# Optimization experiments

Hardware: AMD Instinct MI355X
Metric: run time of the kernel (lower is better)

The kernel has to match this reference:

```python
import jax, jax.numpy as jnp
import numpy as np

B, CIN, T = 32, 64, 4096
E, H, HD, FF, L = 256, 8, 32, 1024, 4
K, S = 15, 2
SEQ = 512
GROUPS = E // 2
EPS = 1e-5


def setup_inputs() -> dict:
    key = jax.random.key(0)
    ks = jax.random.split(key, 16)
    d = {}
    d['x'] = jax.random.normal(ks[0], (B, CIN, T), jnp.float32)
    d['conv0_w'] = jax.random.normal(ks[1], (E, CIN, K), jnp.float32) * 0.03
    d['conv0_b'] = jnp.zeros((E,), jnp.float32)
    d['conv12_w'] = jax.random.normal(ks[2], (2, E, E, K), jnp.float32) * 0.016
    d['conv12_b'] = jnp.zeros((2, E), jnp.float32)
    d['gn_g'] = jnp.ones((3, E), jnp.float32)
    d['gn_b'] = jnp.zeros((3, E), jnp.float32)
    d['Wq'] = jax.random.normal(ks[3], (L, H, HD, E), jnp.float32) * 0.0625
    d['Wk'] = jax.random.normal(ks[4], (L, H, HD, E), jnp.float32) * 0.0625
    d['Wv'] = jax.random.normal(ks[5], (L, H, HD, E), jnp.float32) * 0.0625
    d['Wo'] = jax.random.normal(ks[6], (L, E, E), jnp.float32) * 0.0625
    d['ln1_g'] = jnp.ones((L, E), jnp.float32)
    d['ln1_b'] = jnp.zeros((L, E), jnp.float32)
    d['Wf1'] = jax.random.normal(ks[7], (L, FF, E), jnp.float32) * 0.0625
    d['bf1'] = jnp.zeros((L, FF), jnp.float32)
    d['Wf2'] = jax.random.normal(ks[8], (L, E, FF), jnp.float32) * 0.03125
    d['bf2'] = jnp.zeros((L, E), jnp.float32)
    d['ln2_g'] = jnp.ones((L, E), jnp.float32)
    d['ln2_b'] = jnp.zeros((L, E), jnp.float32)
    d['Wc1'] = jax.random.normal(ks[9], (256, SEQ * E), jnp.float32) * 0.003
    d['bc1'] = jnp.zeros((256,), jnp.float32)
    d['Wc2'] = jax.random.normal(ks[10], (1, 256), jnp.float32) * 0.0625
    d['bc2'] = jnp.zeros((1,), jnp.float32)
    return d


def conv1d(x, w, b, stride, pad):
    y = jax.lax.conv_general_dilated(x, w, (stride,), [(pad, pad)],
                                     dimension_numbers=('NCH', 'OIH', 'NCH'))
    return y + b[None, :, None]


def group_norm(x, g, b):
    # x: [B, C, Len]; torch GroupNorm with C//2 groups
    Bn, C, Ln = x.shape
    xg = x.reshape(Bn, GROUPS, C // GROUPS, Ln)
    mu = xg.mean(axis=(2, 3), keepdims=True)
    var = ((xg - mu) ** 2).mean(axis=(2, 3), keepdims=True)
    xn = ((xg - mu) * jax.lax.rsqrt(var + EPS)).reshape(Bn, C, Ln)
    return xn * g[None, :, None] + b[None, :, None]


def layer_norm(x, g, b):
    mu = x.mean(-1, keepdims=True)
    var = ((x - mu) ** 2).mean(-1, keepdims=True)
    return (x - mu) * jax.lax.rsqrt(var + EPS) * g + b


def pos_encoding(seq, e):
    t = jnp.arange(seq, dtype=jnp.float32)[:, None]
    i = jnp.arange(e, dtype=jnp.float32)[None, :]
    ang = t / jnp.power(10000.0, i / e)  # note: i/e, matching the source
    return jnp.where(jnp.arange(e)[None, :] % 2 == 0, jnp.sin(ang), jnp.cos(ang))


def reference(x, conv0_w, conv0_b, conv12_w, conv12_b, gn_g, gn_b,
              Wq, Wk, Wv, Wo, ln1_g, ln1_b, Wf1, bf1, Wf2, bf2,
              ln2_g, ln2_b, Wc1, bc1, Wc2, bc2):
    # --- conv encoder: (conv -> dropout(eval) -> groupnorm -> gelu) x3 ---
    h = conv1d(x, conv0_w, conv0_b, S, K // 2)
    h = jax.nn.gelu(group_norm(h, gn_g[0], gn_b[0]), approximate=False)
    for i in range(2):
        h = conv1d(h, conv12_w[i], conv12_b[i], S, K // 2)
        h = jax.nn.gelu(group_norm(h, gn_g[i + 1], gn_b[i + 1]), approximate=False)
    h = jnp.transpose(h, (0, 2, 1))  # [B, SEQ, E]

    # --- transformer encoder ---
    h = h + pos_encoding(h.shape[1], E)[None]
    scale = 1.0 / jnp.sqrt(jnp.float32(HD))
    for l in range(L):
        q = jnp.einsum('bse,hde->bhsd', h, Wq[l])
        k = jnp.einsum('bse,hde->bhsd', h, Wk[l])
        v = jnp.einsum('bse,hde->bhsd', h, Wv[l])
        attn = jax.nn.softmax(jnp.einsum('bhqd,bhkd->bhqk', q, k) * scale, axis=-1)
        o = jnp.einsum('bhqk,bhkd->bhqd', attn, v)
        o = jnp.transpose(o, (0, 2, 1, 3)).reshape(h.shape[0], h.shape[1], E)
        o = o @ Wo[l].T
        h1 = layer_norm(o + h, ln1_g[l], ln1_b[l])
        f = jax.nn.relu(h1 @ Wf1[l].T + bf1[l]) @ Wf2[l].T + bf2[l]
        h = layer_norm(f + h1, ln2_g[l], ln2_b[l])

    # --- binary classifier ---
    flat = h.reshape(h.shape[0], -1)  # [B, SEQ*E]
    hid = jax.nn.relu(flat @ Wc1.T + bc1)
    return jax.nn.sigmoid(hid @ Wc2.T + bc2)  # [B, 1]
```

## Files before the change

### kernel.cpp

```cpp
#include <hip/hip_runtime.h>
#include <math.h>


typedef unsigned int   u32;
typedef unsigned short u16;
typedef __attribute__((ext_vector_type(4))) float f32x4;
typedef __attribute__((ext_vector_type(8))) short bf16x8;

#define QSCALE_LOG2E 0.2550348742f

__device__ __forceinline__ u16 f2bf(float v) {
    union { float f; u32 u; } x; x.f = v;
    u32 r = x.u + 0x7fffu + ((x.u >> 16) & 1u);
    return (u16)(r >> 16);
}

__device__ __forceinline__ void gl2lds16(const void* gsrc, void* ldst) {
    __builtin_amdgcn_global_load_lds(
        (const __attribute__((address_space(1))) void*)gsrc,
        (__attribute__((address_space(3))) void*)ldst, 16, 0, 0);
}

__device__ __forceinline__ float maeeg_block_sum(float v, float* sc4) {
#pragma unroll
    for (int off = 32; off; off >>= 1) v += __shfl_down(v, off);
    int t = threadIdx.x;
    if ((t & 63) == 0) sc4[t >> 6] = v;
    __syncthreads();
    float r = sc4[0] + sc4[1] + sc4[2] + sc4[3];
    __syncthreads();
    return r;
}

__global__ __launch_bounds__(256) void maeeg_mm_kernel(
    const u16* __restrict__ Ag, const u16* __restrict__ Bg,
    const float* __restrict__ bias, const float* __restrict__ res,
    void* __restrict__ outp, int N, int K, int flags)
{
    __shared__ u16 As[8192];
    __shared__ u16 Bs[8192];
    const int m0 = blockIdx.x * 128, n0 = blockIdx.y * 128;
    const int t = threadIdx.x, w = t >> 6, lane = t & 63;
    const int fr = lane & 15, fq = lane >> 4;
    const int wm = (w >> 1) * 64, wn = (w & 1) * 64;
    const int srow = lane >> 3;
    const int srcc = (lane & 7) ^ srow;

    f32x4 acc[4][4];
    const f32x4 zero = {0.f, 0.f, 0.f, 0.f};
#pragma unroll
    for (int i = 0; i < 4; ++i)
#pragma unroll
        for (int j = 0; j < 4; ++j) acc[i][j] = zero;

    for (int k0 = 0; k0 < K; k0 += 64) {
#pragma unroll
        for (int j = 0; j < 4; ++j) {
            int rowb = w * 32 + j * 8;
            int r = rowb + srow;
            gl2lds16(Ag + (size_t)(m0 + r) * K + k0 + srcc * 8,
                     (char*)As + rowb * 128);
            gl2lds16(Bg + (size_t)(n0 + r) * K + k0 + srcc * 8,
                     (char*)Bs + rowb * 128);
        }
        __syncthreads();
#pragma unroll
        for (int kc = 0; kc < 2; ++kc) {
            bf16x8 af[4], bfv[4];
#pragma unroll
            for (int i = 0; i < 4; ++i) {
                int am = wm + i * 16 + fr;
                int bn = wn + i * 16 + fr;
                int kb = kc * 64 + fq * 16;
                af[i]  = *(const bf16x8*)((const char*)As + am * 128 + (kb ^ ((am & 7) << 4)));
                bfv[i] = *(const bf16x8*)((const char*)Bs + bn * 128 + (kb ^ ((bn & 7) << 4)));
            }
#pragma unroll
            for (int i = 0; i < 4; ++i)
#pragma unroll
                for (int j = 0; j < 4; ++j)
                    acc[i][j] = __builtin_amdgcn_mfma_f32_16x16x32_bf16(
                        af[i], bfv[j], acc[i][j], 0, 0, 0);
        }
        __syncthreads();
    }
#pragma unroll
    for (int i = 0; i < 4; ++i) {
#pragma unroll
        for (int j = 0; j < 4; ++j) {
            int n = n0 + wn + j * 16 + fr;
            float bv = bias ? bias[n] : 0.f;
#pragma unroll
            for (int r = 0; r < 4; ++r) {
                int m = m0 + wm + i * 16 + fq * 4 + r;
                float v = acc[i][j][r] + bv;
                if (res) v += res[(size_t)m * N + n];
                if (flags & 1) v = fmaxf(v, 0.f);
                if (flags & 16) {
                    u16* o = (u16*)outp;
                    int seg = n >> 8, nn = n & 255;
                    if (seg == 0)
                        o[(size_t)m * 256 + nn] = f2bf(v * QSCALE_LOG2E);
                    else if (seg == 1)
                        o[4194304 + (size_t)m * 256 + nn] = f2bf(v);
                    else
                        o[8388608 + (((size_t)(m >> 9)) * 256 + nn) * 512 + (m & 511)] = f2bf(v);
                } else if (flags & 4)
                    ((u16*)outp)[(((size_t)(m >> 9)) * 256 + n) * 512 + (m & 511)] = f2bf(v);
                else if (flags & 2)
                    ((u16*)outp)[(size_t)m * N + n] = f2bf(v);
                else
                    ((float*)outp)[(size_t)m * N + n] = v;
            }
        }
    }
}

__global__ __launch_bounds__(512) void maeeg_mmln_kernel(
    const u16* __restrict__ Ag, const u16* __restrict__ Bg,
    const float* __restrict__ bias, const float* __restrict__ res,
    const float* __restrict__ g, const float* __restrict__ b,
    float* __restrict__ outf, u16* __restrict__ outb, int K)
{
    __shared__ u16 As[64 * 64];
    __shared__ u16 Bs[256 * 64];
    __shared__ float psum[64][4];
    __shared__ float psq[64][4];
    const int m0 = blockIdx.x * 64;
    const int t = threadIdx.x, w = t >> 6, lane = t & 63;
    const int fr = lane & 15, fq = lane >> 4;
    const int wm = (w & 1) * 32, wn = (w >> 1) * 64;
    const int seg = w >> 1;
    const int srow = lane >> 3;
    const int srcc = (lane & 7) ^ srow;

    f32x4 acc[2][4];
    const f32x4 zero = {0.f, 0.f, 0.f, 0.f};
#pragma unroll
    for (int i = 0; i < 2; ++i)
#pragma unroll
        for (int j = 0; j < 4; ++j) acc[i][j] = zero;

    for (int k0 = 0; k0 < K; k0 += 64) {
        gl2lds16(Ag + (size_t)(m0 + w * 8 + srow) * K + k0 + srcc * 8,
                 (char*)As + (w * 8) * 128);
#pragma unroll
        for (int j = 0; j < 4; ++j) {
            int rowb = w * 32 + j * 8;
            gl2lds16(Bg + (size_t)(rowb + srow) * K + k0 + srcc * 8,
                     (char*)Bs + rowb * 128);
        }
        __syncthreads();
#pragma unroll
        for (int kc = 0; kc < 2; ++kc) {
            int kb = kc * 64 + fq * 16;
            bf16x8 af[2], bfv[4];
#pragma unroll
            for (int i = 0; i < 2; ++i) {
                int am = wm + i * 16 + fr;
                af[i] = *(const bf16x8*)((const char*)As + am * 128 + (kb ^ ((am & 7) << 4)));
            }
#pragma unroll
            for (int j = 0; j < 4; ++j) {
                int bn = wn + j * 16 + fr;
                bfv[j] = *(const bf16x8*)((const char*)Bs + bn * 128 + (kb ^ ((bn & 7) << 4)));
            }
#pragma unroll
            for (int i = 0; i < 2; ++i)
#pragma unroll
                for (int j = 0; j < 4; ++j)
                    acc[i][j] = __builtin_amdgcn_mfma_f32_16x16x32_bf16(
                        af[i], bfv[j], acc[i][j], 0, 0, 0);
        }
        __syncthreads();
    }

#pragma unroll
    for (int j = 0; j < 4; ++j) {
        int n = wn + j * 16 + fr;
        float bv = bias ? bias[n] : 0.f;
#pragma unroll
        for (int i = 0; i < 2; ++i)
#pragma unroll
            for (int r = 0; r < 4; ++r) {
                int m = m0 + wm + i * 16 + fq * 4 + r;
                acc[i][j][r] += bv + res[(size_t)m * 256 + n];
            }
    }
#pragma unroll
    for (int i = 0; i < 2; ++i)
#pragma unroll
        for (int r = 0; r < 4; ++r) {
            float s = acc[i][0][r] + acc[i][1][r] + acc[i][2][r] + acc[i][3][r];
            float q = acc[i][0][r] * acc[i][0][r] + acc[i][1][r] * acc[i][1][r]
                    + acc[i][2][r] * acc[i][2][r] + acc[i][3][r] * acc[i][3][r];
#pragma unroll
            for (int off = 1; off < 16; off <<= 1) {
                s += __shfl_xor(s, off);
                q += __shfl_xor(q, off);
            }
            if (fr == 0) {
                int ml = wm + i * 16 + fq * 4 + r;
                psum[ml][seg] = s;
                psq[ml][seg] = q;
            }
        }
    __syncthreads();
#pragma unroll
    for (int i = 0; i < 2; ++i)
#pragma unroll
        for (int r = 0; r < 4; ++r) {
            int ml = wm + i * 16 + fq * 4 + r;
            float S = psum[ml][0] + psum[ml][1] + psum[ml][2] + psum[ml][3];
            float Q = psq[ml][0] + psq[ml][1] + psq[ml][2] + psq[ml][3];
            float mu = S * (1.f / 256.f);
            float var = fmaxf(Q * (1.f / 256.f) - mu * mu, 0.f);
            float rs = rsqrtf(var + 1e-5f);
            size_t mrow = (size_t)(m0 + ml) * 256;
#pragma unroll
            for (int j = 0; j < 4; ++j) {
                int n = wn + j * 16 + fr;
                float o = (acc[i][j][r] - mu) * rs * g[n] + b[n];
                if (outf) outf[mrow + n] = o;
                outb[mrow + n] = f2bf(o);
            }
        }
}

__global__ __launch_bounds__(256) void maeeg_convmm_kernel(
    const u16* __restrict__ Wp, const u16* __restrict__ inp,
    const float* __restrict__ cb, u16* __restrict__ out,
    int K3, int len_in, int len_out)
{
    __shared__ u16 As[8192];
    __shared__ u16 Bs[8192];
    const int m0 = blockIdx.x * 128, t0 = blockIdx.y * 128, b = blockIdx.z;
    const int lip = len_in + 16;
    const u16* inb = inp + (size_t)b * (K3 >> 4) * lip;
    const int t = threadIdx.x, w = t >> 6, lane = t & 63;
    const int sr = lane & 7, sc = lane >> 3;
    const int fr = lane & 15, fq = lane >> 4;
    const int wm = (w >> 1) * 64, wn = (w & 1) * 64;
    const int srow = lane >> 3;
    const int srcc = (lane & 7) ^ srow;

    f32x4 acc[4][4];
    const f32x4 zero = {0.f, 0.f, 0.f, 0.f};
#pragma unroll
    for (int i = 0; i < 4; ++i)
#pragma unroll
        for (int j = 0; j < 4; ++j) acc[i][j] = zero;

    for (int k0 = 0; k0 < K3; k0 += 64) {
#pragma unroll
        for (int j = 0; j < 4; ++j) {
            int rowb = w * 32 + j * 8;
            gl2lds16(Wp + (size_t)(m0 + rowb + srow) * K3 + k0 + srcc * 8,
                     (char*)As + rowb * 128);
            int row = rowb + sr;
            int k  = k0 + sc * 8;
            int ci = k >> 4, rr = k & 15;
            int tg = t0 + row;
            const u16* gp = inb + (size_t)ci * lip + 2 * tg + rr;
            uint4 vb;
            vb.x = *(const u32*)(gp);
            vb.y = *(const u32*)(gp + 2);
            vb.z = *(const u32*)(gp + 4);
            vb.w = *(const u32*)(gp + 6);
            int kb = (sc ^ (row & 7)) << 4;
            *(uint4*)((char*)Bs + row * 128 + kb) = vb;
        }
        __syncthreads();
#pragma unroll
        for (int kc = 0; kc < 2; ++kc) {
            bf16x8 af[4], bfv[4];
#pragma unroll
            for (int i = 0; i < 4; ++i) {
                int am = wm + i * 16 + fr;
                int bn = wn + i * 16 + fr;
                int kb = kc * 64 + fq * 16;
                af[i]  = *(const bf16x8*)((const char*)As + am * 128 + (kb ^ ((am & 7) << 4)));
                bfv[i] = *(const bf16x8*)((const char*)Bs + bn * 128 + (kb ^ ((bn & 7) << 4)));
            }
#pragma unroll
            for (int i = 0; i < 4; ++i)
#pragma unroll
                for (int j = 0; j < 4; ++j)
                    acc[i][j] = __builtin_amdgcn_mfma_f32_16x16x32_bf16(
                        af[i], bfv[j], acc[i][j], 0, 0, 0);
        }
        __syncthreads();
    }
#pragma unroll
    for (int i = 0; i < 4; ++i) {
#pragma unroll
        for (int r = 0; r < 4; ++r) {
            int m = m0 + wm + i * 16 + fq * 4 + r;
            float bb = cb[m];
            u16* op = out + ((size_t)b * 256 + m) * len_out + t0;
#pragma unroll
            for (int j = 0; j < 4; ++j)
                op[wn + j * 16 + fr] = f2bf(acc[i][j][r] + bb);
        }
    }
}

__global__ __launch_bounds__(256) void maeeg_fattn_kernel(
    const u16* __restrict__ Qb, const u16* __restrict__ Kb,
    const u16* __restrict__ Vt, u16* __restrict__ att)
{
    __shared__ u16 Ks[64 * 32];
    __shared__ u16 Vs[32 * 64];
    __shared__ u16 Ps[4][32 * 64];
    const int qt = blockIdx.x, h = blockIdx.y, b = blockIdx.z;
    const int t = threadIdx.x, w = t >> 6, lane = t & 63;
    const int fr = lane & 15, fq = lane >> 4;
    const u16* qbase = Qb + (size_t)b * 512 * 256 + h * 32;
    const u16* kbase = Kb + (size_t)b * 512 * 256 + h * 32;
    const u16* vbase = Vt + (size_t)b * 256 * 512 + (size_t)h * 32 * 512;

    bf16x8 qf[2];
#pragma unroll
    for (int mi = 0; mi < 2; ++mi)
        qf[mi] = *(const bf16x8*)(qbase +
                 (size_t)(qt * 128 + w * 32 + mi * 16 + fr) * 256 + fq * 8);

    f32x4 oacc[2][2];
    const f32x4 zero = {0.f, 0.f, 0.f, 0.f};
    oacc[0][0] = zero; oacc[0][1] = zero; oacc[1][0] = zero; oacc[1][1] = zero;
    float mrun[8], lrun[8];
#pragma unroll
    for (int i = 0; i < 8; ++i) { mrun[i] = -1e30f; lrun[i] = 0.f; }

    for (int kt = 0; kt < 512; kt += 64) {
        {
            int row = t >> 2, c = t & 3;
            uint4 kv = *(const uint4*)(kbase + (size_t)(kt + row) * 256 + c * 8);
            *(uint4*)((char*)Ks + row * 64 + (((c ^ (row & 3)) << 4))) = kv;
            int d = t >> 3, c2 = t & 7;
            uint4 vv = *(const uint4*)(vbase + (size_t)d * 512 + kt + c2 * 8);
            *(uint4*)((char*)Vs + d * 128 + ((c2 ^ (d & 7)) << 4)) = vv;
        }
        __syncthreads();

        f32x4 sacc[2][4];
#pragma unroll
        for (int mi = 0; mi < 2; ++mi)
#pragma unroll
            for (int ni = 0; ni < 4; ++ni) sacc[mi][ni] = zero;
        bf16x8 kf[4];
#pragma unroll
        for (int ni = 0; ni < 4; ++ni) {
            int kk = ni * 16 + fr;
            kf[ni] = *(const bf16x8*)((const char*)Ks + kk * 64 +
                                      ((fq ^ (kk & 3)) << 4));
        }
#pragma unroll
        for (int mi = 0; mi < 2; ++mi)
#pragma unroll
            for (int ni = 0; ni < 4; ++ni)
                sacc[mi][ni] = __builtin_amdgcn_mfma_f32_16x16x32_bf16(
                    qf[mi], kf[ni], sacc[mi][ni], 0, 0, 0);

#pragma unroll
        for (int mi = 0; mi < 2; ++mi) {
#pragma unroll
            for (int reg = 0; reg < 4; ++reg) {
                int idx = mi * 4 + reg;
                float rm = fmaxf(fmaxf(sacc[mi][0][reg], sacc[mi][1][reg]),
                                 fmaxf(sacc[mi][2][reg], sacc[mi][3][reg]));
                rm = fmaxf(rm, __shfl_xor(rm, 1));
                rm = fmaxf(rm, __shfl_xor(rm, 2));
                rm = fmaxf(rm, __shfl_xor(rm, 4));
                rm = fmaxf(rm, __shfl_xor(rm, 8));
                float mold = mrun[idx];
                float mnew = fmaxf(mold, rm);
                float c = __builtin_amdgcn_exp2f(mold - mnew);
                mrun[idx] = mnew;
                int q = mi * 16 + fq * 4 + reg;
                float psum = 0.f;
#pragma unroll
                for (int ni = 0; ni < 4; ++ni) {
                    float p = __builtin_amdgcn_exp2f(sacc[mi][ni][reg] - mnew);
                    union { float f; u32 u; } px; px.f = p;
                    u32 r16 = (px.u + 0x8000u) >> 16;
                    int kk = ni * 16 + fr;
                    int boff = q * 128 + ((((kk >> 3) ^ (q & 7)) << 4) | ((kk & 7) << 1));
                    *(u16*)((char*)Ps[w] + boff) = (u16)r16;
                    union { u32 u; float f; } pr; pr.u = r16 << 16;
                    psum += pr.f;
                }
                lrun[idx] = lrun[idx] * c + psum;
                oacc[mi][0][reg] *= c;
                oacc[mi][1][reg] *= c;
            }
        }

        bf16x8 pf[2][2], vf[2][2];
#pragma unroll
        for (int mi = 0; mi < 2; ++mi)
#pragma unroll
            for (int kc = 0; kc < 2; ++kc) {
                int q = mi * 16 + fr;
                int ch = (kc * 4 + fq) ^ (q & 7);
                pf[mi][kc] = *(const bf16x8*)((const char*)Ps[w] + q * 128 + (ch << 4));
            }
#pragma unroll
        for (int nj = 0; nj < 2; ++nj)
#pragma unroll
            for (int kc = 0; kc < 2; ++kc) {
                int d = nj * 16 + fr;
                int ch = (kc * 4 + fq) ^ (d & 7);
                vf[nj][kc] = *(const bf16x8*)((const char*)Vs + d * 128 + (ch << 4));
            }
#pragma unroll
        for (int mi = 0; mi < 2; ++mi)
#pragma unroll
            for (int nj = 0; nj < 2; ++nj) {
                oacc[mi][nj] = __builtin_amdgcn_mfma_f32_16x16x32_bf16(
                    pf[mi][0], vf[nj][0], oacc[mi][nj], 0, 0, 0);
                oacc[mi][nj] = __builtin_amdgcn_mfma_f32_16x16x32_bf16(
                    pf[mi][1], vf[nj][1], oacc[mi][nj], 0, 0, 0);
            }
        __syncthreads();
    }

#pragma unroll
    for (int idx = 0; idx < 8; ++idx) {
        float l = lrun[idx];
        l += __shfl_xor(l, 1);
        l += __shfl_xor(l, 2);
        l += __shfl_xor(l, 4);
        l += __shfl_xor(l, 8);
        lrun[idx] = 1.f / l;
    }
    u16* ob = att + (size_t)b * 512 * 256 + h * 32;
#pragma unroll
    for (int mi = 0; mi < 2; ++mi)
#pragma unroll
        for (int reg = 0; reg < 4; ++reg) {
            int q = qt * 128 + w * 32 + mi * 16 + fq * 4 + reg;
            float inv = lrun[mi * 4 + reg];
#pragma unroll
            for (int nj = 0; nj < 2; ++nj)
                ob[(size_t)q * 256 + nj * 16 + fr] =
                    f2bf(oacc[mi][nj][reg] * inv);
        }
}

__global__ void maeeg_prep_convw_kernel(const float* __restrict__ src,
                                        u16* __restrict__ dst, int nrows)
{
    int i = blockIdx.x * 256 + threadIdx.x;
    if (i >= nrows) return;
    const float* s = src + (size_t)i * 15;
    float4 a = *(const float4*)s;
    float4 b = *(const float4*)(s + 4);
    float4 c = *(const float4*)(s + 8);
    float e12 = s[12], e13 = s[13], e14 = s[14];
    uint4 p0, p1;
    p0.x = (u32)f2bf(a.x) | ((u32)f2bf(a.y) << 16);
    p0.y = (u32)f2bf(a.z) | ((u32)f2bf(a.w) << 16);
    p0.z = (u32)f2bf(b.x) | ((u32)f2bf(b.y) << 16);
    p0.w = (u32)f2bf(b.z) | ((u32)f2bf(b.w) << 16);
    p1.x = (u32)f2bf(c.x) | ((u32)f2bf(c.y) << 16);
    p1.y = (u32)f2bf(c.z) | ((u32)f2bf(c.w) << 16);
    p1.z = (u32)f2bf(e12) | ((u32)f2bf(e13) << 16);
    p1.w = (u32)f2bf(e14);
    uint4* d = (uint4*)(dst + (size_t)i * 16);
    d[0] = p0; d[1] = p1;
}

__device__ __forceinline__ uint4 pack8(const float* s) {
    float4 a = ((const float4*)s)[0];
    float4 b = ((const float4*)s)[1];
    uint4 p;
    p.x = (u32)f2bf(a.x) | ((u32)f2bf(a.y) << 16);
    p.y = (u32)f2bf(a.z) | ((u32)f2bf(a.w) << 16);
    p.z = (u32)f2bf(b.x) | ((u32)f2bf(b.y) << 16);
    p.w = (u32)f2bf(b.z) | ((u32)f2bf(b.w) << 16);
    return p;
}

__global__ void maeeg_cast_www_kernel(
    const float* __restrict__ Wo, u16* __restrict__ dWo,
    const float* __restrict__ Wf1, u16* __restrict__ dWf1,
    const float* __restrict__ Wf2, u16* __restrict__ dWf2)
{
    int i = blockIdx.x * 256 + threadIdx.x;
    const float* s; u16* d; int off;
    if (i < 32768)       { s = Wo;  d = dWo;  off = i; }
    else if (i < 163840) { s = Wf1; d = dWf1; off = i - 32768; }
    else                 { s = Wf2; d = dWf2; off = i - 163840; }
    *(uint4*)(d + (size_t)off * 8) = pack8(s + (size_t)off * 8);
}

__global__ void maeeg_cast_qkv3_kernel(
    const float* __restrict__ Wq, const float* __restrict__ Wk,
    const float* __restrict__ Wv, u16* __restrict__ dst)
{
    int seg = blockIdx.y;
    const float* src = (seg == 0) ? Wq : ((seg == 1) ? Wk : Wv);
    int i = blockIdx.x * 256 + threadIdx.x;
    int l = i >> 13, r = (i & 8191) * 8;
    *(uint4*)(dst + (size_t)l * 196608 + seg * 65536 + r) =
        pack8(src + (size_t)i * 8);
}

__global__ void maeeg_cast_pad_kernel(const float* __restrict__ src,
                                      u16* __restrict__ dst, int len)
{
    int lip = len + 16;
    int n8 = lip >> 3;
    int i = blockIdx.x * 256 + threadIdx.x;
    if (i >= n8) return;
    int row = blockIdx.y;
    int p0 = i * 8;
    u16 vals[8];
#pragma unroll
    for (int e = 0; e < 8; ++e) {
        int q = p0 + e - 7;
        vals[e] = (q >= 0 && q < len) ? f2bf(src[(size_t)row * len + q]) : (u16)0;
    }
    uint4 pk;
    pk.x = (u32)vals[0] | ((u32)vals[1] << 16);
    pk.y = (u32)vals[2] | ((u32)vals[3] << 16);
    pk.z = (u32)vals[4] | ((u32)vals[5] << 16);
    pk.w = (u32)vals[6] | ((u32)vals[7] << 16);
    *(uint4*)(dst + (size_t)row * lip + p0) = pk;
}

__global__ void maeeg_pe_kernel(float* __restrict__ pet)
{
    int s = blockIdx.x, e = threadIdx.x;
    float ang = (float)s / powf(10000.f, (float)e * (1.f / 256.f));
    pet[s * 256 + e] = (e & 1) ? cosf(ang) : sinf(ang);
}

__global__ __launch_bounds__(256) void maeeg_gn_gelu_kernel(
    const u16* __restrict__ hin, const float* __restrict__ g,
    const float* __restrict__ bta, int len, u16* __restrict__ bfout, int lip,
    float* __restrict__ f32out)
{
    const int grp = blockIdx.x, b = blockIdx.y;
    const size_t base = ((size_t)b * 256 + grp * 2) * len;
    const u32* p32 = (const u32*)(hin + base);
    float s1 = 0.f, s2 = 0.f;
    for (int i = threadIdx.x; i < len; i += 256) {
        u32 v = p32[i];
        union { u32 u; float f; } lo, hi;
        lo.u = v << 16; hi.u = v & 0xffff0000u;
        s1 += lo.f + hi.f;
        s2 += lo.f * lo.f + hi.f * hi.f;
    }
    __shared__ float sc[4];
    float S1 = maeeg_block_sum(s1, sc);
    float S2 = maeeg_block_sum(s2, sc);
    const float nn = (float)(2 * len);
    float mu = S1 / nn;
    float var = fmaxf(S2 / nn - mu * mu, 0.f);
    float rs = rsqrtf(var + 1e-5f);
    float g0 = g[grp * 2], g1 = g[grp * 2 + 1];
    float b0 = bta[grp * 2], b1 = bta[grp * 2 + 1];
    u16* bp = bfout ? bfout + ((size_t)b * 256 + grp * 2) * lip : (u16*)0;
    float* fp = f32out ? f32out + base : (float*)0;
    for (int i2 = threadIdx.x; i2 < len; i2 += 256) {
        u32 v = p32[i2];
        int i = i2 * 2;
        union { u32 u; float f; } lo, hi;
        lo.u = v << 16; hi.u = v & 0xffff0000u;
        bool c1 = (i >= len);
        float gg = c1 ? g1 : g0, bb = c1 ? b1 : b0;
        float y0 = (lo.f - mu) * rs * gg + bb;
        float y1 = (hi.f - mu) * rs * gg + bb;
        float e0 = 0.5f * y0 * (1.f + erff(y0 * 0.70710678118654752f));
        float e1 = 0.5f * y1 * (1.f + erff(y1 * 0.70710678118654752f));
        if (bp) {
            int j0 = (i < len ? i : i - len + lip) + 7;
            bp[j0] = f2bf(e0);
            bp[j0 + 1] = f2bf(e1);
        }
        if (fp) {
            fp[i] = e0;
            fp[i + 1] = e1;
        }
    }
    if (bp && threadIdx.x < 32) {
        int ch = threadIdx.x >> 4, pp = threadIdx.x & 15;
        bp[(size_t)ch * lip + ((pp < 7) ? pp : (len + pp))] = 0;
    }
}

__global__ __launch_bounds__(256) void maeeg_transpose_pos_kernel(
    const float* __restrict__ in, const float* __restrict__ pet,
    float* __restrict__ out, u16* __restrict__ outb)
{
    __shared__ float tile[256][33];
    const int s0 = blockIdx.x * 32, b = blockIdx.y;
    for (int idx = threadIdx.x; idx < 256 * 32; idx += 256) {
        int e = idx >> 5, j = idx & 31;
        tile[e][j] = in[((size_t)b * 256 + e) * 512 + s0 + j];
    }
    __syncthreads();
    for (int idx = threadIdx.x; idx < 32 * 256; idx += 256) {
        int j = idx >> 8, e = idx & 255;
        float v = tile[e][j] + pet[(s0 + j) * 256 + e];
        size_t o = ((size_t)b * 512 + s0 + j) * 256 + e;
        out[o] = v;
        outb[o] = f2bf(v);
    }
}

__global__ __launch_bounds__(256) void maeeg_cls1_kernel(
    const u16* __restrict__ flatb, const float* __restrict__ Wc1,
    float* __restrict__ part)
{
    __shared__ u16 As[32 * 64];
    __shared__ u16 Bs[64 * 64];
    const int ks = blockIdx.x, jt = blockIdx.y;
    const int t = threadIdx.x, w = t >> 6, lane = t & 63;
    const int fr = lane & 15, fq = lane >> 4;
    const int kbase0 = ks * 512;
    const int brow = t >> 2, bq = t & 3;
    const int srow = lane >> 3;
    const int srcc = (lane & 7) ^ srow;

    f32x4 acc[2];
    const f32x4 zero = {0.f, 0.f, 0.f, 0.f};
    acc[0] = zero; acc[1] = zero;

    for (int step = 0; step < 8; ++step) {
        int kk = kbase0 + step * 64;
        int rowb = w * 8;
        gl2lds16(flatb + (size_t)(rowb + srow) * 131072 + kk + srcc * 8,
                 (char*)As + rowb * 128);
        const float* wp = Wc1 + (size_t)(jt * 64 + brow) * 131072 + kk + bq * 16;
        float4 f0 = ((const float4*)wp)[0];
        float4 f1 = ((const float4*)wp)[1];
        float4 f2 = ((const float4*)wp)[2];
        float4 f3 = ((const float4*)wp)[3];
        uint4 p0, p1;
        p0.x = (u32)f2bf(f0.x) | ((u32)f2bf(f0.y) << 16);
        p0.y = (u32)f2bf(f0.z) | ((u32)f2bf(f0.w) << 16);
        p0.z = (u32)f2bf(f1.x) | ((u32)f2bf(f1.y) << 16);
        p0.w = (u32)f2bf(f1.z) | ((u32)f2bf(f1.w) << 16);
        p1.x = (u32)f2bf(f2.x) | ((u32)f2bf(f2.y) << 16);
        p1.y = (u32)f2bf(f2.z) | ((u32)f2bf(f2.w) << 16);
        p1.z = (u32)f2bf(f3.x) | ((u32)f2bf(f3.y) << 16);
        p1.w = (u32)f2bf(f3.z) | ((u32)f2bf(f3.w) << 16);
        int c0 = bq * 2, c1 = bq * 2 + 1;
        *(uint4*)((char*)Bs + brow * 128 + ((c0 ^ (brow & 7)) << 4)) = p0;
        *(uint4*)((char*)Bs + brow * 128 + ((c1 ^ (brow & 7)) << 4)) = p1;
        __syncthreads();
#pragma unroll
        for (int kc = 0; kc < 2; ++kc) {
            int kbyte = kc * 64 + fq * 16;
            int bn = w * 16 + fr;
            bf16x8 bfv = *(const bf16x8*)((const char*)Bs + bn * 128 +
                                          (kbyte ^ ((bn & 7) << 4)));
#pragma unroll
            for (int mi = 0; mi < 2; ++mi) {
                int am = mi * 16 + fr;
                bf16x8 af = *(const bf16x8*)((const char*)As + am * 128 +
                                             (kbyte ^ ((am & 7) << 4)));
                acc[mi] = __builtin_amdgcn_mfma_f32_16x16x32_bf16(
                    af, bfv, acc[mi], 0, 0, 0);
            }
        }
        __syncthreads();
    }
#pragma unroll
    for (int mi = 0; mi < 2; ++mi)
#pragma unroll
        for (int r = 0; r < 4; ++r) {
            int m = mi * 16 + fq * 4 + r;
            int j = jt * 64 + w * 16 + fr;
            part[((size_t)ks * 32 + m) * 256 + j] = acc[mi][r];
        }
}

__global__ __launch_bounds__(256) void maeeg_cls23_kernel(
    const float* __restrict__ part, const float* __restrict__ bc1,
    const float* __restrict__ Wc2, const float* __restrict__ bc2,
    float* __restrict__ out)
{
    const int b = blockIdx.x, j = threadIdx.x;
    float s = bc1[j];
    for (int ks = 0; ks < 256; ++ks) s += part[((size_t)ks * 32 + b) * 256 + j];
    float v = fmaxf(s, 0.f) * Wc2[j];
    __shared__ float sc[4];
    float tot = maeeg_block_sum(v, sc);
    if (j == 0) out[b] = 1.f / (1.f + expf(-(tot + bc2[0])));
}

extern "C" void kernel_launch(void* const* d_in, const int* in_sizes, int n_in,
                              void* d_out, int out_size, void* d_ws, size_t ws_size,
                              hipStream_t stream)
{
    (void)in_sizes; (void)n_in; (void)out_size; (void)ws_size;
    const float* x        = (const float*)d_in[0];
    const float* conv0_w  = (const float*)d_in[1];
    const float* conv0_b  = (const float*)d_in[2];
    const float* conv12_w = (const float*)d_in[3];
    const float* conv12_b = (const float*)d_in[4];
    const float* gn_g     = (const float*)d_in[5];
    const float* gn_b     = (const float*)d_in[6];
    const float* Wq       = (const float*)d_in[7];
    const float* Wk       = (const float*)d_in[8];
    const float* Wv       = (const float*)d_in[9];
    const float* Wo       = (const float*)d_in[10];
    const float* ln1_g    = (const float*)d_in[11];
    const float* ln1_b    = (const float*)d_in[12];
    const float* Wf1      = (const float*)d_in[13];
    const float* bf1      = (const float*)d_in[14];
    const float* Wf2      = (const float*)d_in[15];
    const float* bf2      = (const float*)d_in[16];
    const float* ln2_g    = (const float*)d_in[17];
    const float* ln2_b    = (const float*)d_in[18];
    const float* Wc1      = (const float*)d_in[19];
    const float* bc1      = (const float*)d_in[20];
    const float* Wc2      = (const float*)d_in[21];
    const float* bc2      = (const float*)d_in[22];
    float* out = (float*)d_out;

    char* wsb = (char*)d_ws;
    u16* WB0   = (u16*)(wsb + 0);
    u16* WB12  = (u16*)(wsb + 524288);
    u16* WQKVb = (u16*)(wsb + 4718592);
    u16* WOb   = (u16*)(wsb + 6291456);
    u16* WF1b  = (u16*)(wsb + 6815744);
    u16* WF2b  = (u16*)(wsb + 8912896);
    u16*   XPAD  = (u16*)(wsb + 11010048);
    u16*   GN1B  = (u16*)(wsb + 11010048);
    float* D     = (float*)(wsb + 11010048);
    u16*   CONV0B = (u16*)(wsb + 28049408);
    u16*   CONV1B = (u16*)(wsb + 28049408);
    u16*   CONV2B = (u16*)(wsb + 28049408 + 33554432);
    float* GN2F   = (float*)(wsb + 28049408);
    u16*   Qb2   = (u16*)(wsb + 28049408);
    u16*   ATTb  = (u16*)(wsb + 28049408 + 25165824);
    u16*   Db    = (u16*)(wsb + 28049408 + 33554432);
    u16*   F1b   = (u16*)(wsb + 28049408);
    float* PART  = (float*)(wsb + 28049408);
    u16*   GN0B  = (u16*)(wsb + 95158272);
    float* C     = (float*)(wsb + 95158272);
    u16*   Cb    = (u16*)(wsb + 95158272 + 16777216);
    float* PET   = (float*)(wsb + 133201920);

    maeeg_prep_convw_kernel<<<64, 256, 0, stream>>>(conv0_w, WB0, 16384);
    maeeg_prep_convw_kernel<<<512, 256, 0, stream>>>(conv12_w, WB12, 131072);
    maeeg_cast_qkv3_kernel<<<dim3(128, 3), 256, 0, stream>>>(Wq, Wk, Wv, WQKVb);
    maeeg_cast_www_kernel<<<1152, 256, 0, stream>>>(Wo, WOb, Wf1, WF1b, Wf2, WF2b);
    maeeg_cast_pad_kernel<<<dim3(3, 2048), 256, 0, stream>>>(x, XPAD, 4096);
    maeeg_pe_kernel<<<512, 256, 0, stream>>>(PET);

    maeeg_convmm_kernel<<<dim3(2, 16, 32), 256, 0, stream>>>(
        WB0, XPAD, conv0_b, CONV0B, 1024, 4096, 2048);
    maeeg_gn_gelu_kernel<<<dim3(128, 32), 256, 0, stream>>>(
        CONV0B, gn_g, gn_b, 2048, GN0B, 2064, (float*)0);
    maeeg_convmm_kernel<<<dim3(2, 8, 32), 256, 0, stream>>>(
        WB12, GN0B, conv12_b, CONV1B, 4096, 2048, 1024);
    maeeg_gn_gelu_kernel<<<dim3(128, 32), 256, 0, stream>>>(
        CONV1B, gn_g + 256, gn_b + 256, 1024, GN1B, 1040, (float*)0);
    maeeg_convmm_kernel<<<dim3(2, 4, 32), 256, 0, stream>>>(
        WB12 + 256 * 4096, GN1B, conv12_b + 256, CONV2B, 4096, 1024, 512);
    maeeg_gn_gelu_kernel<<<dim3(128, 32), 256, 0, stream>>>(
        CONV2B, gn_g + 512, gn_b + 512, 512, (u16*)0, 0, GN2F);
    maeeg_transpose_pos_kernel<<<dim3(16, 32), 256, 0, stream>>>(GN2F, PET, C, Cb);

    for (int l = 0; l < 4; ++l) {
        maeeg_mm_kernel<<<dim3(128, 6), 256, 0, stream>>>(
            Cb, WQKVb + l * 196608, (const float*)0, (const float*)0,
            Qb2, 256, 256, 16);
        maeeg_fattn_kernel<<<dim3(4, 8, 32), 256, 0, stream>>>(
            Qb2, Qb2 + 4194304, Qb2 + 8388608, ATTb);
        maeeg_mmln_kernel<<<256, 512, 0, stream>>>(
            ATTb, WOb + l * 65536, (const float*)0, C,
            ln1_g + l * 256, ln1_b + l * 256, D, Db, 256);
        maeeg_mm_kernel<<<dim3(128, 8), 256, 0, stream>>>(
            Db, WF1b + l * 262144, bf1 + l * 1024, (const float*)0, F1b, 1024, 256, 3);
        maeeg_mmln_kernel<<<256, 512, 0, stream>>>(
            F1b, WF2b + l * 262144, bf2 + l * 256, D,
            ln2_g + l * 256, ln2_b + l * 256, (l == 3) ? (float*)0 : C, Cb, 1024);
    }

    maeeg_cls1_kernel<<<dim3(256, 4), 256, 0, stream>>>(Cb, Wc1, PART);
    maeeg_cls23_kernel<<<32, 256, 0, stream>>>(PART, bc1, Wc2, bc2, out);
}
```

Before: 913.5 us.

## Load conv GEMM fragments directly from global memory, skip LDS staging

The conv-as-GEMM kernel no longer stages A and B tiles through shared memory with barriers. Each lane now loads its MFMA fragments straight from global memory (relying on L1/L2 for reuse) and advances pointers per k-step. Separately, the attention kernel raises wave priority around its MFMA blocks. This removes LDS traffic and syncs, but it increases redundant global/cache loads because operands are no longer shared across waves.

```diff
diff --git a/kernel.cpp b/kernel.cpp
--- a/kernel.cpp
+++ b/kernel.cpp
@@ -232,17 +232,14 @@
     const float* __restrict__ cb, u16* __restrict__ out,
     int K3, int len_in, int len_out)
 {
-    __shared__ u16 As[8192];
-    __shared__ u16 Bs[8192];
     const int m0 = blockIdx.x * 128, t0 = blockIdx.y * 128, b = blockIdx.z;
     const int lip = len_in + 16;
     const u16* inb = inp + (size_t)b * (K3 >> 4) * lip;
     const int t = threadIdx.x, w = t >> 6, lane = t & 63;
-    const int sr = lane & 7, sc = lane >> 3;
     const int fr = lane & 15, fq = lane >> 4;
     const int wm = (w >> 1) * 64, wn = (w & 1) * 64;
-    const int srow = lane >> 3;
-    const int srcc = (lane & 7) ^ srow;
+    const int r0  = (fq & 1) * 8;
+    const int cib = fq >> 1;
 
     f32x4 acc[4][4];
     const f32x4 zero = {0.f, 0.f, 0.f, 0.f};
@@ -251,45 +248,47 @@
 #pragma unroll
         for (int j = 0; j < 4; ++j) acc[i][j] = zero;
 
+    const u16* ap[4];
+    const u16* bp[4];
+#pragma unroll
+    for (int i = 0; i < 4; ++i) {
+        ap[i] = Wp + (size_t)(m0 + wm + i * 16 + fr) * K3 + fq * 8;
+        bp[i] = inb + (size_t)cib * lip + 2 * (t0 + wn + i * 16 + fr) + r0;
+    }
+
     for (int k0 = 0; k0 < K3; k0 += 64) {
-#pragma unroll
-        for (int j = 0; j < 4; ++j) {
-            int rowb = w * 32 + j * 8;
-            gl2lds16(Wp + (size_t)(m0 + rowb + srow) * K3 + k0 + srcc * 8,
-                     (char*)As + rowb * 128);
-            int row = rowb + sr;
-            int k  = k0 + sc * 8;
-            int ci = k >> 4, rr = k & 15;
-            int tg = t0 + row;
-            const u16* gp = inb + (size_t)ci * lip + 2 * tg + rr;
-            uint4 vb;
-            vb.x = *(const u32*)(gp);
-            vb.y = *(const u32*)(gp + 2);
-            vb.z = *(const u32*)(gp + 4);
-            vb.w = *(const u32*)(gp + 6);
-            int kb = (sc ^ (row & 7)) << 4;
-            *(uint4*)((char*)Bs + row * 128 + kb) = vb;
-        }
-        __syncthreads();
-#pragma unroll
-        for (int kc = 0; kc < 2; ++kc) {
-            bf16x8 af[4], bfv[4];
+        bf16x8 af[2][4];
+        uint4  bu[2][4];
+#pragma unroll
+        for (int kc = 0; kc < 2; ++kc)
+#pragma unroll
+            for (int i = 0; i < 4; ++i)
+                af[kc][i] = *(const bf16x8*)(ap[i] + kc * 32);
+#pragma unroll
+        for (int kc = 0; kc < 2; ++kc)
 #pragma unroll
             for (int i = 0; i < 4; ++i) {
-                int am = wm + i * 16 + fr;
-                int bn = wn + i * 16 + fr;
-                int kb = kc * 64 + fq * 16;
-                af[i]  = *(const bf16x8*)((const char*)As + am * 128 + (kb ^ ((am & 7) << 4)));
-                bfv[i] = *(const bf16x8*)((const char*)Bs + bn * 128 + (kb ^ ((bn & 7) << 4)));
-            }
+                const u16* gp = bp[i] + (size_t)(kc * 2) * lip;
+                uint4 v;
+                v.x = *(const u32*)(gp);
+                v.y = *(const u32*)(gp + 2);
+                v.z = *(const u32*)(gp + 4);
+                v.w = *(const u32*)(gp + 6);
+                bu[kc][i] = v;
+            }
+#pragma unroll
+        for (int kc = 0; kc < 2; ++kc)
 #pragma unroll
             for (int i = 0; i < 4; ++i)
 #pragma unroll
                 for (int j = 0; j < 4; ++j)
                     acc[i][j] = __builtin_amdgcn_mfma_f32_16x16x32_bf16(
-                        af[i], bfv[j], acc[i][j], 0, 0, 0);
-        }
-        __syncthreads();
+                        af[kc][i], *(const bf16x8*)&bu[kc][j], acc[i][j], 0, 0, 0);
+#pragma unroll
+        for (int i = 0; i < 4; ++i) {
+            ap[i] += 64;
+            bp[i] += 4 * (size_t)lip;
+        }
     }
 #pragma unroll
     for (int i = 0; i < 4; ++i) {
@@ -355,12 +354,14 @@
             kf[ni] = *(const bf16x8*)((const char*)Ks + kk * 64 +
                                       ((fq ^ (kk & 3)) << 4));
         }
+        __builtin_amdgcn_s_setprio(1);
 #pragma unroll
         for (int mi = 0; mi < 2; ++mi)
 #pragma unroll
             for (int ni = 0; ni < 4; ++ni)
                 sacc[mi][ni] = __builtin_amdgcn_mfma_f32_16x16x32_bf16(
                     qf[mi], kf[ni], sacc[mi][ni], 0, 0, 0);
+        __builtin_amdgcn_s_setprio(0);
 
 #pragma unroll
         for (int mi = 0; mi < 2; ++mi) {
@@ -413,6 +414,7 @@
                 int ch = (kc * 4 + fq) ^ (d & 7);
                 vf[nj][kc] = *(const bf16x8*)((const char*)Vs + d * 128 + (ch << 4));
             }
+        __builtin_amdgcn_s_setprio(1);
 #pragma unroll
         for (int mi = 0; mi < 2; ++mi)
 #pragma unroll
@@ -422,6 +424,7 @@
                 oacc[mi][nj] = __builtin_amdgcn_mfma_f32_16x16x32_bf16(
                     pf[mi][1], vf[nj][1], oacc[mi][nj], 0, 0, 0);
             }
+        __builtin_amdgcn_s_setprio(0);
         __syncthreads();
     }
 
```

Measured after the change: 1.002 ms. +9.7%, slower.
